# Performance work log

Measured on AMD Instinct MI355X. Metric: run time of the kernel, lower is better.

Reference implementation:

```python
import jax, jax.numpy as jnp
import numpy as np
from jax import lax

DIM = 512
HEADS = 8


def _branch(x, w1, wd):
    # 1x1 pointwise conv (no bias)
    y = jnp.einsum('oc,bchw->bohw', w1, x)
    # ReflectionPad2d(2)
    y = jnp.pad(y, ((0, 0), (0, 0), (2, 2), (2, 2)), mode='reflect')
    # depthwise 3x3, dilation 2, valid padding (net: same spatial size)
    y = lax.conv_general_dilated(
        y, wd, window_strides=(1, 1), padding='VALID', rhs_dilation=(2, 2),
        dimension_numbers=('NCHW', 'OIHW', 'NCHW'), feature_group_count=y.shape[1])
    return y


def setup_inputs() -> dict:
    key = jax.random.key(0)
    ks = jax.random.split(key, 8)
    s = 0.02
    style_feat = jax.random.normal(ks[0], (16, DIM, 64, 64), dtype=jnp.float32)
    fw1 = jax.random.normal(ks[1], (DIM, DIM), dtype=jnp.float32) * s
    fwd_ = jax.random.normal(ks[2], (DIM, 1, 3, 3), dtype=jnp.float32) * s
    gw1 = jax.random.normal(ks[3], (DIM, DIM), dtype=jnp.float32) * s
    gwd = jax.random.normal(ks[4], (DIM, 1, 3, 3), dtype=jnp.float32) * s
    hw1 = jax.random.normal(ks[5], (DIM, DIM), dtype=jnp.float32) * s
    hwd = jax.random.normal(ks[6], (DIM, 1, 3, 3), dtype=jnp.float32) * s
    ow = jax.random.normal(ks[7], (DIM, DIM), dtype=jnp.float32) * s
    temperature = jnp.ones((HEADS, 1, 1), dtype=jnp.float32)
    return dict(style_feat=style_feat, fw1=fw1, fwd_=fwd_, gw1=gw1, gwd=gwd,
                hw1=hw1, hwd=hwd, ow=ow, temperature=temperature)


def reference(style_feat, fw1, fwd_, gw1, gwd, hw1, hwd, ow, temperature):
    B, C, H, W = style_feat.shape
    cph = C // HEADS
    f_x = _branch(style_feat, fw1, fwd_)
    g_x = _branch(style_feat, gw1, gwd)
    h_x = _branch(style_feat, hw1, hwd)
    q = f_x.reshape(B, HEADS, cph, H * W)
    k = g_x.reshape(B, HEADS, cph, H * W)
    v = h_x.reshape(B, HEADS, cph, H * W)
    # channel-wise attention: [B,h,cph,cph]
    energy = jnp.einsum('bhcn,bhdn->bhcd', q, k)
    attn = jax.nn.softmax(energy * temperature[None], axis=-1)
    out = jnp.einsum('bhcd,bhdn->bhcn', attn, v).reshape(B, C, H, W)
    out = jnp.einsum('oc,bchw->bohw', ow, out)
    return out + style_feat
```

## Files before the change

### kernel.cpp

```cpp
#include <hip/hip_runtime.h>

typedef unsigned short u16;
typedef __bf16 bf8_t __attribute__((ext_vector_type(8)));
typedef short short8 __attribute__((ext_vector_type(8)));
typedef u16 u16x4 __attribute__((ext_vector_type(4)));
typedef float f32x4 __attribute__((ext_vector_type(4)));

#define DEV __device__ __forceinline__

DEV u16 f2bf(float x) {
  unsigned u = __builtin_bit_cast(unsigned, x);
  return (u16)((u + 0x7FFFu + ((u >> 16) & 1u)) >> 16);
}
DEV float bf2f(u16 x) {
  unsigned u = (unsigned)x << 16;
  return __builtin_bit_cast(float, u);
}

DEV void gload16(const u16* g, u16* l) {
  __builtin_amdgcn_global_load_lds((__attribute__((address_space(1))) void*)(g),
                                   (__attribute__((address_space(3))) void*)(l), 16, 0, 0);
}

__global__ void k_wconv(const float* __restrict__ f, const float* __restrict__ g,
                        const float* __restrict__ h, u16* __restrict__ out) {
  int i4 = (blockIdx.x * 256 + threadIdx.x) * 4;
  const float* src = (i4 < 262144) ? (f + i4) : (i4 < 524288) ? (g + i4 - 262144) : (h + i4 - 524288);
  f32x4 v = *(const f32x4*)src;
  u16x4 o;
#pragma unroll
  for (int e = 0; e < 4; ++e) o[e] = f2bf(v[e]);
  *(u16x4*)(out + i4) = o;
}

__global__ __launch_bounds__(256) void k_xt(const float* __restrict__ style, u16* __restrict__ Xt) {
  __shared__ float t[32][33];
  int b = blockIdx.z, c0 = blockIdx.y * 32, n0 = blockIdx.x * 32;
  int tid = threadIdx.x, lr = tid >> 5, lc = tid & 31;
  const float* src = style + ((size_t)b * 512 + c0) * 4096 + n0;
#pragma unroll
  for (int it = 0; it < 4; ++it) {
    int r = it * 8 + lr;
    t[r][lc] = src[(size_t)r * 4096 + lc];
  }
  __syncthreads();
  u16* dst = Xt + ((size_t)b * 4096 + n0) * 512 + c0;
#pragma unroll
  for (int it = 0; it < 4; ++it) {
    int n = it * 8 + lr;
    dst[(size_t)n * 512 + lc] = f2bf(t[lc][n]);
  }
}

DEV void stage_tile(const u16* __restrict__ src, int row0, int kb,
                    u16* lds, int wave, int lane) {
#pragma unroll
  for (int qq = 0; qq < 2; ++qq) {
    int idx = (wave * 2 + qq) * 64 + lane;
    int r = idx >> 2;
    int cb = (idx & 3) * 8;
    gload16(src + (size_t)(row0 + r) * 512 + (kb + cb),
            lds + (wave * 2 + qq) * 512);
  }
}

__global__ __launch_bounds__(256, 2) void k_gemm_branch(
    const u16* __restrict__ Wall, const u16* __restrict__ Xt, u16* __restrict__ Y) {
  int z = blockIdx.z;
  int t = z >> 4, b = z & 15;
  int M0 = t * 512 + blockIdx.y * 128, N0 = blockIdx.x * 128;
  const u16* A = Wall;
  const u16* B = Xt + (size_t)b * (4096 * 512);
  u16* C = Y + (size_t)b * (1536 * 4096);
  int tid = threadIdx.x, wave = tid >> 6, lane = tid & 63;
  int wm = wave >> 1, wn = wave & 1;
  __shared__ __align__(16) u16 lA[2][128 * 32];
  __shared__ __align__(16) u16 lB[2][128 * 32];
  f32x4 acc[4][4];
#pragma unroll
  for (int m = 0; m < 4; ++m)
#pragma unroll
    for (int n = 0; n < 4; ++n) acc[m][n] = (f32x4){0.f, 0.f, 0.f, 0.f};
  stage_tile(A, M0, 0, &lA[0][0], wave, lane);
  stage_tile(B, N0, 0, &lB[0][0], wave, lane);
  __syncthreads();
  int lrow = lane & 15, lk = (lane >> 4) * 8;
#pragma unroll 2
  for (int kt = 0; kt < 16; ++kt) {
    int cur = kt & 1;
    if (kt < 15) {
      stage_tile(A, M0, (kt + 1) * 32, &lA[cur ^ 1][0], wave, lane);
      stage_tile(B, N0, (kt + 1) * 32, &lB[cur ^ 1][0], wave, lane);
    }
    bf8_t af[4], bff[4];
#pragma unroll
    for (int m = 0; m < 4; ++m)
      af[m] = *(const bf8_t*)&lA[cur][(wm * 64 + m * 16 + lrow) * 32 + lk];
#pragma unroll
    for (int n = 0; n < 4; ++n)
      bff[n] = *(const bf8_t*)&lB[cur][(wn * 64 + n * 16 + lrow) * 32 + lk];
#pragma unroll
    for (int m = 0; m < 4; ++m)
#pragma unroll
      for (int n = 0; n < 4; ++n)
        acc[m][n] = __builtin_amdgcn_mfma_f32_16x16x32_bf16(af[m], bff[n], acc[m][n], 0, 0, 0);
    __syncthreads();
  }
  int orow = (lane >> 4) * 4, ocol = lane & 15;
#pragma unroll
  for (int m = 0; m < 4; ++m)
#pragma unroll
    for (int n = 0; n < 4; ++n) {
      int row = M0 + wm * 64 + m * 16 + orow;
      int col = N0 + wn * 64 + n * 16 + ocol;
      u16* cp = C + (size_t)row * 4096 + col;
#pragma unroll
      for (int i = 0; i < 4; ++i) cp[(size_t)i * 4096] = f2bf(acc[m][n][i]);
    }
}

template <typename F>
DEV void dw_row(const u16* plane, const float* w9, int y, F&& store) {
  short8 raw[3][8];
#pragma unroll
  for (int i = 0; i < 3; ++i) {
    int yy = y + 2 * i - 2;
    yy = yy < 0 ? -yy : (yy > 63 ? 126 - yy : yy);
    const short8* rp = (const short8*)(plane + yy * 64);
#pragma unroll
    for (int ch = 0; ch < 8; ++ch) raw[i][ch] = rp[ch];
  }
#pragma unroll
  for (int g = 0; g < 4; ++g) {
    float fr[3][20];
#pragma unroll
    for (int t = 0; t < 20; ++t) {
      int p = g * 16 - 2 + t;
      int rp2 = p < 0 ? -p : (p > 63 ? 126 - p : p);
#pragma unroll
      for (int i = 0; i < 3; ++i)
        fr[i][t] = bf2f((u16)raw[i][rp2 >> 3][rp2 & 7]);
    }
    float o[16];
#pragma unroll
    for (int e = 0; e < 16; ++e) {
      float s = 0.f;
#pragma unroll
      for (int i = 0; i < 3; ++i)
#pragma unroll
        for (int j = 0; j < 3; ++j)
          s += w9[i * 3 + j] * fr[i][e + 2 * j];
      o[e] = s;
    }
    store(g, o);
  }
}

__global__ __launch_bounds__(256, 2) void k_dwE(const u16* __restrict__ Y,
    const float* __restrict__ fwd, const float* __restrict__ gwd, float* __restrict__ E) {
  int band = blockIdx.x, h = blockIdx.y, b = blockIdx.z;
  __shared__ __align__(16) u16 qbuf[64 * 256];
  __shared__ __align__(16) u16 kbuf[64 * 256];
  int tid = threadIdx.x;
  int c = ((tid >> 5) << 3) | (tid & 7);
  int yl = (tid >> 3) & 3;
  int wv = tid >> 6, lane = tid & 63;
  int lrow = lane & 15, lkg = lane >> 4;
  const u16* qp = Y + ((size_t)b * 1536 + h * 64 + c) * 4096;
  const u16* kp = Y + ((size_t)b * 1536 + 512 + h * 64 + c) * 4096;
  float wq9[9], wk9[9];
#pragma unroll
  for (int t = 0; t < 9; ++t) {
    wq9[t] = fwd[(h * 64 + c) * 9 + t];
    wk9[t] = gwd[(h * 64 + c) * 9 + t];
  }
  f32x4 acc[4];
#pragma unroll
  for (int n = 0; n < 4; ++n) acc[n] = (f32x4){0.f, 0.f, 0.f, 0.f};
  char* qrow = (char*)qbuf + c * 512;
  char* krow = (char*)kbuf + c * 512;
  int c7 = c & 7;
#pragma unroll 1
  for (int sb = 0; sb < 4; ++sb) {
    int y = band * 16 + sb * 4 + yl;
    dw_row(qp, wq9, y, [&](int g, const float* o) {
      short8 s0, s1;
#pragma unroll
      for (int e = 0; e < 8; ++e) { s0[e] = (short)f2bf(o[e]); s1[e] = (short)f2bf(o[e + 8]); }
      int ch0 = yl * 8 + g * 2;
      *(short8*)(qrow + 16 * (ch0 ^ c7)) = s0;
      *(short8*)(qrow + 16 * ((ch0 + 1) ^ c7)) = s1;
    });
    dw_row(kp, wk9, y, [&](int g, const float* o) {
      short8 s0, s1;
#pragma unroll
      for (int e = 0; e < 8; ++e) { s0[e] = (short)f2bf(o[e]); s1[e] = (short)f2bf(o[e + 8]); }
      int ch0 = yl * 8 + g * 2;
      *(short8*)(krow + 16 * (ch0 ^ c7)) = s0;
      *(short8*)(krow + 16 * ((ch0 + 1) ^ c7)) = s1;
    });
    __syncthreads();
    const char* qb = (const char*)qbuf + (wv * 16 + lrow) * 512;
    int ca7 = (wv * 16 + lrow) & 7;
#pragma unroll
    for (int ks = 0; ks < 8; ++ks) {
      bf8_t aF = *(const bf8_t*)(qb + 16 * ((ks * 4 + lkg) ^ ca7));
#pragma unroll
      for (int n = 0; n < 4; ++n) {
        int cb = n * 16 + lrow;
        bf8_t bF = *(const bf8_t*)((const char*)kbuf + cb * 512 + 16 * ((ks * 4 + lkg) ^ (cb & 7)));
        acc[n] = __builtin_amdgcn_mfma_f32_16x16x32_bf16(aF, bF, acc[n], 0, 0, 0);
      }
    }
    __syncthreads();
  }
  float* Eo = E + (((size_t)band * 16 + b) * 8 + h) * 4096;
  int orow = (lane >> 4) * 4, ocol = lane & 15;
#pragma unroll
  for (int n = 0; n < 4; ++n)
#pragma unroll
    for (int i = 0; i < 4; ++i)
      Eo[(wv * 16 + orow + i) * 64 + n * 16 + ocol] = acc[n][i];
}

__global__ __launch_bounds__(256, 2) void k_dwV(const u16* __restrict__ Y,
    const float* __restrict__ hwd, u16* __restrict__ Vt) {
  int band = blockIdx.x, ct = blockIdx.y, b = blockIdx.z;
  __shared__ float vb[256 * 68];
  int tid = threadIdx.x;
  int c = ((tid >> 5) << 3) | (tid & 7);
  int yl = (tid >> 3) & 3;
  int cg = tid & 7;
  int cglob = ct * 64 + c;
  const u16* plane = Y + ((size_t)b * 1536 + 1024 + cglob) * 4096;
  float w9[9];
#pragma unroll
  for (int t = 0; t < 9; ++t) w9[t] = hwd[cglob * 9 + t];
#pragma unroll 1
  for (int sb = 0; sb < 4; ++sb) {
    int y = band * 16 + sb * 4 + yl;
    dw_row(plane, w9, y, [&](int g, const float* o) {
#pragma unroll
      for (int e = 0; e < 16; ++e)
        vb[((g * 16 + e) * 4 + yl) * 68 + c] = o[e];
    });
    __syncthreads();
#pragma unroll
    for (int k = 0; k < 8; ++k) {
      int np = (tid >> 3) + 32 * k;
      int x = np >> 2, yy = np & 3;
      int ng = (band * 16 + sb * 4 + yy) * 64 + x;
      f32x4 r0 = *(const f32x4*)&vb[np * 68 + cg * 8];
      f32x4 r1 = *(const f32x4*)&vb[np * 68 + cg * 8 + 4];
      short8 s;
#pragma unroll
      for (int e = 0; e < 4; ++e) { s[e] = (short)f2bf(r0[e]); s[e + 4] = (short)f2bf(r1[e]); }
      *(short8*)(Vt + ((size_t)b * 4096 + ng) * 512 + ct * 64 + cg * 8) = s;
    }
    __syncthreads();
  }
}

__global__ __launch_bounds__(64) void k_softmax(float* __restrict__ E, const float* __restrict__ temp) {
  int bh = blockIdx.x;
  int b = bh >> 3, h = bh & 7;
  int c = threadIdx.x;
  float* p0 = E + (((size_t)b * 8 + h) * 64 + c) * 64;
  float tv = temp[h];
  float e[64];
  float mx = -1e30f;
#pragma unroll
  for (int d = 0; d < 64; ++d) {
    float v = (p0[d] + p0[d + 524288] + p0[d + 1048576] + p0[d + 1572864]) * tv;
    e[d] = v;
    mx = fmaxf(mx, v);
  }
  float s = 0.f;
#pragma unroll
  for (int d = 0; d < 64; ++d) { float v = __expf(e[d] - mx); e[d] = v; s += v; }
  float inv = 1.f / s;
#pragma unroll
  for (int d = 0; d < 64; ++d) p0[d] = e[d] * inv;
}

__global__ __launch_bounds__(256) void k_m2(const float* __restrict__ E, const float* __restrict__ ow,
                                            u16* __restrict__ M2) {
  int og = blockIdx.x, h = blockIdx.y, b = blockIdx.z;
  __shared__ float at[4096];
  int tid = threadIdx.x;
  const float* attn = E + ((size_t)b * 8 + h) * 4096;
  for (int v = tid; v < 4096; v += 256) at[v] = attn[v];
  __syncthreads();
  int o = og * 64 + (tid >> 2), dq = (tid & 3) * 16;
  const float* owr = ow + (size_t)o * 512 + h * 64;
  float acc[16];
#pragma unroll
  for (int e = 0; e < 16; ++e) acc[e] = 0.f;
  for (int cc = 0; cc < 64; ++cc) {
    float wv = owr[cc];
#pragma unroll
    for (int e = 0; e < 16; ++e) acc[e] += wv * at[cc * 64 + dq + e];
  }
  u16* dst = M2 + ((size_t)b * 512 + o) * 512 + h * 64 + dq;
  short8 s0, s1;
#pragma unroll
  for (int e = 0; e < 8; ++e) { s0[e] = (short)f2bf(acc[e]); s1[e] = (short)f2bf(acc[e + 8]); }
  *(short8*)dst = s0;
  *(short8*)(dst + 8) = s1;
}

__global__ __launch_bounds__(256, 2) void k_gemm_final(
    const u16* __restrict__ M2, const u16* __restrict__ Vt,
    const float* __restrict__ style, float* __restrict__ out) {
  int b = blockIdx.z;
  const u16* A = M2 + (size_t)b * (512 * 512);
  const u16* B = Vt + (size_t)b * (4096 * 512);
  const float* st = style + (size_t)b * (512 * 4096);
  float* op = out + (size_t)b * (512 * 4096);
  int M0 = blockIdx.y * 128, N0 = blockIdx.x * 128;
  int tid = threadIdx.x, wave = tid >> 6, lane = tid & 63;
  int wm = wave >> 1, wn = wave & 1;
  __shared__ __align__(16) u16 lA[2][128 * 32];
  __shared__ __align__(16) u16 lB[2][128 * 32];
  f32x4 acc[4][4];
#pragma unroll
  for (int m = 0; m < 4; ++m)
#pragma unroll
    for (int n = 0; n < 4; ++n) acc[m][n] = (f32x4){0.f, 0.f, 0.f, 0.f};
  stage_tile(A, M0, 0, &lA[0][0], wave, lane);
  stage_tile(B, N0, 0, &lB[0][0], wave, lane);
  __syncthreads();
  int lrow = lane & 15, lk = (lane >> 4) * 8;
#pragma unroll 2
  for (int kt = 0; kt < 16; ++kt) {
    int cur = kt & 1;
    if (kt < 15) {
      stage_tile(A, M0, (kt + 1) * 32, &lA[cur ^ 1][0], wave, lane);
      stage_tile(B, N0, (kt + 1) * 32, &lB[cur ^ 1][0], wave, lane);
    }
    bf8_t af[4], bff[4];
#pragma unroll
    for (int m = 0; m < 4; ++m)
      af[m] = *(const bf8_t*)&lA[cur][(wm * 64 + m * 16 + lrow) * 32 + lk];
#pragma unroll
    for (int n = 0; n < 4; ++n)
      bff[n] = *(const bf8_t*)&lB[cur][(wn * 64 + n * 16 + lrow) * 32 + lk];
#pragma unroll
    for (int m = 0; m < 4; ++m)
#pragma unroll
      for (int n = 0; n < 4; ++n)
        acc[m][n] = __builtin_amdgcn_mfma_f32_16x16x32_bf16(af[m], bff[n], acc[m][n], 0, 0, 0);
    __syncthreads();
  }
  int orow = (lane >> 4) * 4, ocol = lane & 15;
#pragma unroll
  for (int m = 0; m < 4; ++m)
#pragma unroll
    for (int n = 0; n < 4; ++n) {
      int row = M0 + wm * 64 + m * 16 + orow;
      int col = N0 + wn * 64 + n * 16 + ocol;
      float* cp = op + (size_t)row * 4096 + col;
      const float* sp = st + (size_t)row * 4096 + col;
#pragma unroll
      for (int i = 0; i < 4; ++i) cp[(size_t)i * 4096] = acc[m][n][i] + sp[(size_t)i * 4096];
    }
}


extern "C" void kernel_launch(void* const* d_in, const int* in_sizes, int n_in,
                              void* d_out, int out_size, void* d_ws, size_t ws_size,
                              hipStream_t stream) {
  const float* style = (const float*)d_in[0];
  const float* fw1   = (const float*)d_in[1];
  const float* fwd_  = (const float*)d_in[2];
  const float* gw1   = (const float*)d_in[3];
  const float* gwd   = (const float*)d_in[4];
  const float* hw1   = (const float*)d_in[5];
  const float* hwd   = (const float*)d_in[6];
  const float* ow    = (const float*)d_in[7];
  const float* temp  = (const float*)d_in[8];
  float* out = (float*)d_out;

  char* ws = (char*)d_ws;
  u16*   Wbf = (u16*)(ws + 0);
  u16*   Y   = (u16*)(ws + (size_t)2097152);
  u16*   Xt  = (u16*)(ws + (size_t)203423744);
  u16*   Vt  = Xt;
  float* E   = (float*)(ws + (size_t)270532608);
  u16*   M2  = (u16*)(ws + (size_t)278921216);

  k_wconv<<<768, 256, 0, stream>>>(fw1, gw1, hw1, Wbf);
  k_xt<<<dim3(128, 16, 16), 256, 0, stream>>>(style, Xt);
  k_gemm_branch<<<dim3(32, 4, 48), 256, 0, stream>>>(Wbf, Xt, Y);
  k_dwE<<<dim3(4, 8, 16), 256, 0, stream>>>(Y, fwd_, gwd, E);
  k_dwV<<<dim3(4, 8, 16), 256, 0, stream>>>(Y, hwd, Vt);
  k_softmax<<<128, 64, 0, stream>>>(E, temp);
  k_m2<<<dim3(8, 8, 16), 256, 0, stream>>>(E, ow, M2);
  k_gemm_final<<<dim3(32, 4, 16), 256, 0, stream>>>(M2, Vt, style, out);
}
```

Before: 404.2 us.

## Fuse style transpose/bf16 conversion into branch GEMM with resident swizzled B tile

Removes the separate transpose kernel and has the branch GEMM load fp32 style columns directly, converting to bf16 into an XOR-swizzled LDS buffer holding all 512 channels for a 64-pixel strip. Each block then loops over all 12 M tiles of the stacked weights, streaming only A tiles. This saves a full write and read of the transposed activation, but it shrinks the N tile to 64, adds a 64KB+ LDS footprint that limits occupancy, and leaves a serial fp32 load prologue. Each block also restages the whole 1536x512 weight matrix.

```diff
diff --git a/kernel.cpp b/kernel.cpp
--- a/kernel.cpp
+++ b/kernel.cpp
@@ -33,25 +33,6 @@
   *(u16x4*)(out + i4) = o;
 }
 
-__global__ __launch_bounds__(256) void k_xt(const float* __restrict__ style, u16* __restrict__ Xt) {
-  __shared__ float t[32][33];
-  int b = blockIdx.z, c0 = blockIdx.y * 32, n0 = blockIdx.x * 32;
-  int tid = threadIdx.x, lr = tid >> 5, lc = tid & 31;
-  const float* src = style + ((size_t)b * 512 + c0) * 4096 + n0;
-#pragma unroll
-  for (int it = 0; it < 4; ++it) {
-    int r = it * 8 + lr;
-    t[r][lc] = src[(size_t)r * 4096 + lc];
-  }
-  __syncthreads();
-  u16* dst = Xt + ((size_t)b * 4096 + n0) * 512 + c0;
-#pragma unroll
-  for (int it = 0; it < 4; ++it) {
-    int n = it * 8 + lr;
-    dst[(size_t)n * 512 + lc] = f2bf(t[lc][n]);
-  }
-}
-
 DEV void stage_tile(const u16* __restrict__ src, int row0, int kb,
                     u16* lds, int wave, int lane) {
 #pragma unroll
@@ -64,59 +45,79 @@
   }
 }
 
-__global__ __launch_bounds__(256, 2) void k_gemm_branch(
-    const u16* __restrict__ Wall, const u16* __restrict__ Xt, u16* __restrict__ Y) {
-  int z = blockIdx.z;
-  int t = z >> 4, b = z & 15;
-  int M0 = t * 512 + blockIdx.y * 128, N0 = blockIdx.x * 128;
-  const u16* A = Wall;
-  const u16* B = Xt + (size_t)b * (4096 * 512);
+__global__ __launch_bounds__(256, 2) void k_gemm_direct(
+    const u16* __restrict__ Wall, const float* __restrict__ style, u16* __restrict__ Y) {
+  int n0 = blockIdx.x * 64, b = blockIdx.y;
   u16* C = Y + (size_t)b * (1536 * 4096);
   int tid = threadIdx.x, wave = tid >> 6, lane = tid & 63;
   int wm = wave >> 1, wn = wave & 1;
-  __shared__ __align__(16) u16 lA[2][128 * 32];
-  __shared__ __align__(16) u16 lB[2][128 * 32];
-  f32x4 acc[4][4];
+  int lrow = lane & 15, lk = (lane >> 4) * 8;
+
+  __shared__ __align__(16) u16 Bp[64 * 512];
+  __shared__ __align__(16) u16 Ad[2][128 * 32];
+
+  {
+    const float* sp = style + (size_t)b * 512 * 4096 + n0;
+#pragma unroll 1
+    for (int it = 0; it < 32; ++it) {
+      int id = it * 256 + tid;
+      int c = id >> 4, f4 = id & 15;
+      f32x4 v = *(const f32x4*)(sp + (size_t)c * 4096 + f4 * 4);
+#pragma unroll
+      for (int j = 0; j < 4; ++j) {
+        int nl = f4 * 4 + j;
+        int byte = nl * 1024 + (((c >> 3) ^ (nl & 7)) << 4) + (c & 7) * 2;
+        *(u16*)((char*)Bp + byte) = f2bf(v[j]);
+      }
+    }
+  }
+  stage_tile(Wall, 0, 0, &Ad[0][0], wave, lane);
+  __syncthreads();
+
+  f32x4 acc[4][2];
 #pragma unroll
   for (int m = 0; m < 4; ++m)
 #pragma unroll
-    for (int n = 0; n < 4; ++n) acc[m][n] = (f32x4){0.f, 0.f, 0.f, 0.f};
-  stage_tile(A, M0, 0, &lA[0][0], wave, lane);
-  stage_tile(B, N0, 0, &lB[0][0], wave, lane);
-  __syncthreads();
-  int lrow = lane & 15, lk = (lane >> 4) * 8;
-#pragma unroll 2
-  for (int kt = 0; kt < 16; ++kt) {
-    int cur = kt & 1;
-    if (kt < 15) {
-      stage_tile(A, M0, (kt + 1) * 32, &lA[cur ^ 1][0], wave, lane);
-      stage_tile(B, N0, (kt + 1) * 32, &lB[cur ^ 1][0], wave, lane);
-    }
-    bf8_t af[4], bff[4];
+    for (int n = 0; n < 2; ++n) acc[m][n] = (f32x4){0.f, 0.f, 0.f, 0.f};
+
+  int orow = (lane >> 4) * 4, ocol = lane & 15;
+#pragma unroll 1
+  for (int s = 0; s < 192; ++s) {
+    int mt = s >> 4, kt = s & 15, cur = s & 1;
+    if (s < 191) {
+      int sn = s + 1;
+      stage_tile(Wall, (sn >> 4) * 128, (sn & 15) * 32, &Ad[cur ^ 1][0], wave, lane);
+    }
+    bf8_t af[4], bf[2];
 #pragma unroll
     for (int m = 0; m < 4; ++m)
-      af[m] = *(const bf8_t*)&lA[cur][(wm * 64 + m * 16 + lrow) * 32 + lk];
-#pragma unroll
-    for (int n = 0; n < 4; ++n)
-      bff[n] = *(const bf8_t*)&lB[cur][(wn * 64 + n * 16 + lrow) * 32 + lk];
+      af[m] = *(const bf8_t*)&Ad[cur][(wm * 64 + m * 16 + lrow) * 32 + lk];
+#pragma unroll
+    for (int n = 0; n < 2; ++n) {
+      int nl = wn * 32 + n * 16 + lrow;
+      int g = kt * 4 + (lk >> 3);
+      bf[n] = *(const bf8_t*)((const char*)Bp + nl * 1024 + ((g ^ (nl & 7)) << 4));
+    }
 #pragma unroll
     for (int m = 0; m < 4; ++m)
 #pragma unroll
-      for (int n = 0; n < 4; ++n)
-        acc[m][n] = __builtin_amdgcn_mfma_f32_16x16x32_bf16(af[m], bff[n], acc[m][n], 0, 0, 0);
-    __syncthreads();
-  }
-  int orow = (lane >> 4) * 4, ocol = lane & 15;
-#pragma unroll
-  for (int m = 0; m < 4; ++m)
-#pragma unroll
-    for (int n = 0; n < 4; ++n) {
-      int row = M0 + wm * 64 + m * 16 + orow;
-      int col = N0 + wn * 64 + n * 16 + ocol;
-      u16* cp = C + (size_t)row * 4096 + col;
-#pragma unroll
-      for (int i = 0; i < 4; ++i) cp[(size_t)i * 4096] = f2bf(acc[m][n][i]);
-    }
+      for (int n = 0; n < 2; ++n)
+        acc[m][n] = __builtin_amdgcn_mfma_f32_16x16x32_bf16(af[m], bf[n], acc[m][n], 0, 0, 0);
+    if (kt == 15) {
+#pragma unroll
+      for (int m = 0; m < 4; ++m)
+#pragma unroll
+        for (int n = 0; n < 2; ++n) {
+          int row = mt * 128 + wm * 64 + m * 16 + orow;
+          int col = n0 + wn * 32 + n * 16 + ocol;
+          u16* cp = C + (size_t)row * 4096 + col;
+#pragma unroll
+          for (int i = 0; i < 4; ++i) cp[(size_t)i * 4096] = f2bf(acc[m][n][i]);
+          acc[m][n] = (f32x4){0.f, 0.f, 0.f, 0.f};
+        }
+    }
+    __syncthreads();
+  }
 }
 
 template <typename F>
@@ -307,6 +308,18 @@
   for (int e = 0; e < 8; ++e) { s0[e] = (short)f2bf(acc[e]); s1[e] = (short)f2bf(acc[e + 8]); }
   *(short8*)dst = s0;
   *(short8*)(dst + 8) = s1;
+}
+
+DEV void stage_tile_f(const u16* __restrict__ src, int row0, int kb,
+                      u16* lds, int wave, int lane) {
+#pragma unroll
+  for (int qq = 0; qq < 2; ++qq) {
+    int idx = (wave * 2 + qq) * 64 + lane;
+    int r = idx >> 2;
+    int cb = (idx & 3) * 8;
+    gload16(src + (size_t)(row0 + r) * 512 + (kb + cb),
+            lds + (wave * 2 + qq) * 512);
+  }
 }
 
 __global__ __launch_bounds__(256, 2) void k_gemm_final(
@@ -327,16 +340,16 @@
   for (int m = 0; m < 4; ++m)
 #pragma unroll
     for (int n = 0; n < 4; ++n) acc[m][n] = (f32x4){0.f, 0.f, 0.f, 0.f};
-  stage_tile(A, M0, 0, &lA[0][0], wave, lane);
-  stage_tile(B, N0, 0, &lB[0][0], wave, lane);
+  stage_tile_f(A, M0, 0, &lA[0][0], wave, lane);
+  stage_tile_f(B, N0, 0, &lB[0][0], wave, lane);
   __syncthreads();
   int lrow = lane & 15, lk = (lane >> 4) * 8;
 #pragma unroll 2
   for (int kt = 0; kt < 16; ++kt) {
     int cur = kt & 1;
     if (kt < 15) {
-      stage_tile(A, M0, (kt + 1) * 32, &lA[cur ^ 1][0], wave, lane);
-      stage_tile(B, N0, (kt + 1) * 32, &lB[cur ^ 1][0], wave, lane);
+      stage_tile_f(A, M0, (kt + 1) * 32, &lA[cur ^ 1][0], wave, lane);
+      stage_tile_f(B, N0, (kt + 1) * 32, &lB[cur ^ 1][0], wave, lane);
     }
     bf8_t af[4], bff[4];
 #pragma unroll
@@ -384,14 +397,12 @@
   char* ws = (char*)d_ws;
   u16*   Wbf = (u16*)(ws + 0);
   u16*   Y   = (u16*)(ws + (size_t)2097152);
-  u16*   Xt  = (u16*)(ws + (size_t)203423744);
-  u16*   Vt  = Xt;
+  u16*   Vt  = (u16*)(ws + (size_t)203423744);
   float* E   = (float*)(ws + (size_t)270532608);
   u16*   M2  = (u16*)(ws + (size_t)278921216);
 
   k_wconv<<<768, 256, 0, stream>>>(fw1, gw1, hw1, Wbf);
-  k_xt<<<dim3(128, 16, 16), 256, 0, stream>>>(style, Xt);
-  k_gemm_branch<<<dim3(32, 4, 48), 256, 0, stream>>>(Wbf, Xt, Y);
+  k_gemm_direct<<<dim3(64, 16), 256, 0, stream>>>(Wbf, style, Y);
   k_dwE<<<dim3(4, 8, 16), 256, 0, stream>>>(Y, fwd_, gwd, E);
   k_dwV<<<dim3(4, 8, 16), 256, 0, stream>>>(Y, hwd, Vt);
   k_softmax<<<128, 64, 0, stream>>>(E, temp);
```

Result: slower. 460.7 us (+14.0%).

## Pre-swizzle branch weights into MFMA fragment order and load A directly

Applied to the files above, without the earlier changes.

The weight-conversion kernel now writes the three 1x1 conv weights in bf16, already arranged in the per-lane MFMA fragment order. The branch GEMM then reads its A operand straight from global memory (through cache) as contiguous 16-byte loads, instead of staging it through LDS. This removes half the LDS staging traffic and the A-side LDS footprint. In exchange, the global loads of A sit on the critical path without double-buffered prefetch. The final GEMM only switches to a duplicated copy of the staging helper.

```diff
diff --git a/kernel.cpp b/kernel.cpp
--- a/kernel.cpp
+++ b/kernel.cpp
@@ -22,15 +22,21 @@
                                    (__attribute__((address_space(3))) void*)(l), 16, 0, 0);
 }
 
-__global__ void k_wconv(const float* __restrict__ f, const float* __restrict__ g,
-                        const float* __restrict__ h, u16* __restrict__ out) {
-  int i4 = (blockIdx.x * 256 + threadIdx.x) * 4;
-  const float* src = (i4 < 262144) ? (f + i4) : (i4 < 524288) ? (g + i4 - 262144) : (h + i4 - 524288);
-  f32x4 v = *(const f32x4*)src;
-  u16x4 o;
-#pragma unroll
-  for (int e = 0; e < 4; ++e) o[e] = f2bf(v[e]);
-  *(u16x4*)(out + i4) = o;
+__global__ void k_waw(const float* __restrict__ f, const float* __restrict__ g,
+                      const float* __restrict__ h, u16* __restrict__ AW) {
+  int cid = blockIdx.x * 256 + threadIdx.x;
+  int lane = cid & 63, m = (cid >> 6) & 3, wm = (cid >> 8) & 1;
+  int kt = (cid >> 9) & 15, mt = cid >> 13;
+  int row = mt * 128 + wm * 64 + m * 16 + (lane & 15);
+  int col = kt * 32 + (lane >> 4) * 8;
+  int t = row >> 9, rr = row & 511;
+  const float* src = (t == 0 ? f : t == 1 ? g : h) + (size_t)rr * 512 + col;
+  f32x4 v0 = *(const f32x4*)src;
+  f32x4 v1 = *(const f32x4*)(src + 4);
+  short8 s;
+#pragma unroll
+  for (int e = 0; e < 4; ++e) { s[e] = (short)f2bf(v0[e]); s[e + 4] = (short)f2bf(v1[e]); }
+  *(short8*)(AW + (size_t)cid * 8) = s;
 }
 
 __global__ __launch_bounds__(256) void k_xt(const float* __restrict__ style, u16* __restrict__ Xt) {
@@ -65,37 +71,32 @@
 }
 
 __global__ __launch_bounds__(256, 2) void k_gemm_branch(
-    const u16* __restrict__ Wall, const u16* __restrict__ Xt, u16* __restrict__ Y) {
+    const u16* __restrict__ AW, const u16* __restrict__ Xt, u16* __restrict__ Y) {
   int z = blockIdx.z;
   int t = z >> 4, b = z & 15;
-  int M0 = t * 512 + blockIdx.y * 128, N0 = blockIdx.x * 128;
-  const u16* A = Wall;
+  int mt = t * 4 + blockIdx.y;
+  int N0 = blockIdx.x * 128;
   const u16* B = Xt + (size_t)b * (4096 * 512);
   u16* C = Y + (size_t)b * (1536 * 4096);
   int tid = threadIdx.x, wave = tid >> 6, lane = tid & 63;
   int wm = wave >> 1, wn = wave & 1;
-  __shared__ __align__(16) u16 lA[2][128 * 32];
   __shared__ __align__(16) u16 lB[2][128 * 32];
   f32x4 acc[4][4];
 #pragma unroll
   for (int m = 0; m < 4; ++m)
 #pragma unroll
     for (int n = 0; n < 4; ++n) acc[m][n] = (f32x4){0.f, 0.f, 0.f, 0.f};
-  stage_tile(A, M0, 0, &lA[0][0], wave, lane);
   stage_tile(B, N0, 0, &lB[0][0], wave, lane);
   __syncthreads();
   int lrow = lane & 15, lk = (lane >> 4) * 8;
 #pragma unroll 2
   for (int kt = 0; kt < 16; ++kt) {
     int cur = kt & 1;
-    if (kt < 15) {
-      stage_tile(A, M0, (kt + 1) * 32, &lA[cur ^ 1][0], wave, lane);
-      stage_tile(B, N0, (kt + 1) * 32, &lB[cur ^ 1][0], wave, lane);
-    }
+    if (kt < 15) stage_tile(B, N0, (kt + 1) * 32, &lB[cur ^ 1][0], wave, lane);
+    const u16* ab = AW + (size_t)((mt * 16 + kt) * 2 + wm) * 2048 + lane * 8;
     bf8_t af[4], bff[4];
 #pragma unroll
-    for (int m = 0; m < 4; ++m)
-      af[m] = *(const bf8_t*)&lA[cur][(wm * 64 + m * 16 + lrow) * 32 + lk];
+    for (int m = 0; m < 4; ++m) af[m] = *(const bf8_t*)(ab + m * 512);
 #pragma unroll
     for (int n = 0; n < 4; ++n)
       bff[n] = *(const bf8_t*)&lB[cur][(wn * 64 + n * 16 + lrow) * 32 + lk];
@@ -111,7 +112,7 @@
   for (int m = 0; m < 4; ++m)
 #pragma unroll
     for (int n = 0; n < 4; ++n) {
-      int row = M0 + wm * 64 + m * 16 + orow;
+      int row = mt * 128 + wm * 64 + m * 16 + orow;
       int col = N0 + wn * 64 + n * 16 + ocol;
       u16* cp = C + (size_t)row * 4096 + col;
 #pragma unroll
@@ -307,6 +308,18 @@
   for (int e = 0; e < 8; ++e) { s0[e] = (short)f2bf(acc[e]); s1[e] = (short)f2bf(acc[e + 8]); }
   *(short8*)dst = s0;
   *(short8*)(dst + 8) = s1;
+}
+
+DEV void stage_tile_f(const u16* __restrict__ src, int row0, int kb,
+                      u16* lds, int wave, int lane) {
+#pragma unroll
+  for (int qq = 0; qq < 2; ++qq) {
+    int idx = (wave * 2 + qq) * 64 + lane;
+    int r = idx >> 2;
+    int cb = (idx & 3) * 8;
+    gload16(src + (size_t)(row0 + r) * 512 + (kb + cb),
+            lds + (wave * 2 + qq) * 512);
+  }
 }
 
 __global__ __launch_bounds__(256, 2) void k_gemm_final(
@@ -327,16 +340,16 @@
   for (int m = 0; m < 4; ++m)
 #pragma unroll
     for (int n = 0; n < 4; ++n) acc[m][n] = (f32x4){0.f, 0.f, 0.f, 0.f};
-  stage_tile(A, M0, 0, &lA[0][0], wave, lane);
-  stage_tile(B, N0, 0, &lB[0][0], wave, lane);
+  stage_tile_f(A, M0, 0, &lA[0][0], wave, lane);
+  stage_tile_f(B, N0, 0, &lB[0][0], wave, lane);
   __syncthreads();
   int lrow = lane & 15, lk = (lane >> 4) * 8;
 #pragma unroll 2
   for (int kt = 0; kt < 16; ++kt) {
     int cur = kt & 1;
     if (kt < 15) {
-      stage_tile(A, M0, (kt + 1) * 32, &lA[cur ^ 1][0], wave, lane);
-      stage_tile(B, N0, (kt + 1) * 32, &lB[cur ^ 1][0], wave, lane);
+      stage_tile_f(A, M0, (kt + 1) * 32, &lA[cur ^ 1][0], wave, lane);
+      stage_tile_f(B, N0, (kt + 1) * 32, &lB[cur ^ 1][0], wave, lane);
     }
     bf8_t af[4], bff[4];
 #pragma unroll
@@ -382,16 +395,16 @@
   float* out = (float*)d_out;
 
   char* ws = (char*)d_ws;
-  u16*   Wbf = (u16*)(ws + 0);
+  u16*   AW  = (u16*)(ws + 0);
   u16*   Y   = (u16*)(ws + (size_t)2097152);
   u16*   Xt  = (u16*)(ws + (size_t)203423744);
   u16*   Vt  = Xt;
   float* E   = (float*)(ws + (size_t)270532608);
   u16*   M2  = (u16*)(ws + (size_t)278921216);
 
-  k_wconv<<<768, 256, 0, stream>>>(fw1, gw1, hw1, Wbf);
+  k_waw<<<384, 256, 0, stream>>>(fw1, gw1, hw1, AW);
   k_xt<<<dim3(128, 16, 16), 256, 0, stream>>>(style, Xt);
-  k_gemm_branch<<<dim3(32, 4, 48), 256, 0, stream>>>(Wbf, Xt, Y);
+  k_gemm_branch<<<dim3(32, 4, 48), 256, 0, stream>>>(AW, Xt, Y);
   k_dwE<<<dim3(4, 8, 16), 256, 0, stream>>>(Y, fwd_, gwd, E);
   k_dwV<<<dim3(4, 8, 16), 256, 0, stream>>>(Y, hwd, Vt);
   k_softmax<<<128, 64, 0, stream>>>(E, temp);
```

Result: slower. 413.4 us (+2.3%).
